# Kernel tuning notes

Measured on AMD Instinct MI355X. Metric: run time of the kernel, lower is better.

The kernel has to match this reference:

```python
import jax, jax.numpy as jnp
import numpy as np

N_NODES = 100000
K_NEIGH = 16
C = 128
B = 1


def setup_inputs() -> dict:
    key = jax.random.key(0)
    k1, k2, k3, k4, k5, k6 = jax.random.split(key, 6)
    inp = jax.random.normal(k1, (B, C, N_NODES), dtype=jnp.float32)
    adj = jax.random.randint(k2, (N_NODES, K_NEIGH), 0, N_NODES)
    w1 = jax.random.normal(k3, (C, C), dtype=jnp.float32) * 0.05
    b1 = jax.random.normal(k4, (C,), dtype=jnp.float32) * 0.05
    w2 = jax.random.normal(k5, (C, C), dtype=jnp.float32) * 0.05
    b2 = jax.random.normal(k6, (C,), dtype=jnp.float32) * 0.05
    return {"input": inp, "adj": adj, "w1": w1, "b1": b1, "w2": w2, "b2": b2}


def reference(input, adj, w1, b1, w2, b2):
    # fc1: 1x1 conv == channel-mixing matmul. input: [B, C, N]
    state_in = jnp.einsum('oc,bcn->bon', w1, input) + b1[None, :, None]
    # gather neighbor features: [B, C, N, K], mean over neighbors -> [B, C, N]
    neigh = input[:, :, adj]            # [B, C, N, K]
    agg = neigh.mean(axis=3)            # [B, C, N]
    fwd = jnp.einsum('oc,bcn->bon', w2, agg) + b2[None, :, None]
    return state_in + fwd
```

## Files before the change

### kernel.cpp

```cpp
#include <hip/hip_runtime.h>
#include <stdint.h>

#define N_NODES 100000
#define CH 128
#define K_NEIGH 16
#define TN 32
#define XT_STRIDE 36
#define XS_STRIDE 68
#define PS 132

#define PSWZ(n, o) ((n) * PS + ((o) ^ ((((n) >> 3) & 3) << 3)))


__device__ __forceinline__ uint32_t pack_bf16x2(float a, float b) {
    union { float f; uint32_t u; } ua, ub;
    ua.f = a; ub.f = b;
    const uint32_t ra = (ua.u + 0x7fffu + ((ua.u >> 16) & 1u)) >> 16;
    const uint32_t rb = (ub.u + 0x7fffu + ((ub.u >> 16) & 1u)) >> 16;
    return ra | (rb << 16);
}
__device__ __forceinline__ float bf16_lo(uint32_t u) {
    union { uint32_t u; float f; } c; c.u = u << 16; return c.f;
}
__device__ __forceinline__ float bf16_hi(uint32_t u) {
    union { uint32_t u; float f; } c; c.u = u & 0xffff0000u; return c.f;
}

__global__ __launch_bounds__(256, 8) void k_w2x_t(
    const float*  __restrict__ X,
    const float*  __restrict__ W2,
    uint16_t*     __restrict__ Yt)
{
    __shared__ __align__(16) float Xs[CH * XT_STRIDE];

    const int t  = threadIdx.x;
    const int n0 = blockIdx.x * TN;

    for (int it = 0; it < 4; ++it) {
        const int idx = t + it * 256;
        const int nq = idx & 7, c = idx >> 3;
        *(float4*)&Xs[c * XT_STRIDE + nq * 4] =
            *(const float4*)&X[(size_t)c * N_NODES + n0 + nq * 4];
    }
    __syncthreads();

    const int ng = t & 7, og = t >> 3;
    float acc[4][4];
#pragma unroll
    for (int i = 0; i < 4; ++i)
#pragma unroll
        for (int j = 0; j < 4; ++j) acc[i][j] = 0.0f;

    const float* wp = W2 + (size_t)(og * 4) * CH;
#pragma unroll 1
    for (int c0 = 0; c0 < CH; c0 += 4) {
        float4 wq[4];
#pragma unroll
        for (int i = 0; i < 4; ++i)
            wq[i] = *(const float4*)&wp[i * CH + c0];
#pragma unroll
        for (int e = 0; e < 4; ++e) {
            const float4 xv = *(const float4*)&Xs[(c0 + e) * XT_STRIDE + ng * 4];
#pragma unroll
            for (int i = 0; i < 4; ++i) {
                const float w = ((const float*)&wq[i])[e];
                acc[i][0] = fmaf(w, xv.x, acc[i][0]);
                acc[i][1] = fmaf(w, xv.y, acc[i][1]);
                acc[i][2] = fmaf(w, xv.z, acc[i][2]);
                acc[i][3] = fmaf(w, xv.w, acc[i][3]);
            }
        }
    }

#pragma unroll
    for (int j = 0; j < 4; ++j) {
        const int n = n0 + ng * 4 + j;
        uint2 v;
        v.x = pack_bf16x2(acc[0][j], acc[1][j]);
        v.y = pack_bf16x2(acc[2][j], acc[3][j]);
        *(uint2*)&Yt[(size_t)n * CH + og * 4] = v;
    }
}

__global__ __launch_bounds__(256, 8) void k_main(
    const float*    __restrict__ X,
    const int*      __restrict__ adj,
    const float*    __restrict__ W1,
    const float*    __restrict__ B1,
    const float*    __restrict__ B2,
    const uint16_t* __restrict__ Yt,
    float*          __restrict__ Out)
{
    __shared__ __align__(16) float Xs[CH * XT_STRIDE];
    __shared__ __align__(16) int adjS[TN * K_NEIGH];

    const int t  = threadIdx.x;
    const int n0 = blockIdx.x * TN;

    if (t < 128)
        *(int4*)&adjS[t * 4] = *(const int4*)&adj[(size_t)n0 * K_NEIGH + t * 4];
    for (int it = 0; it < 4; ++it) {
        const int idx = t + it * 256;
        const int nq = idx & 7, c = idx >> 3;
        *(float4*)&Xs[c * XT_STRIDE + nq * 4] =
            *(const float4*)&X[(size_t)c * N_NODES + n0 + nq * 4];
    }
    __syncthreads();

    const int ng = t & 7, og = t >> 3;
    float acc[4][4];
#pragma unroll
    for (int i = 0; i < 4; ++i)
#pragma unroll
        for (int j = 0; j < 4; ++j) acc[i][j] = 0.0f;

    const float* wp = W1 + (size_t)(og * 4) * CH;
#pragma unroll 1
    for (int c0 = 0; c0 < CH; c0 += 4) {
        float4 wq[4];
#pragma unroll
        for (int i = 0; i < 4; ++i)
            wq[i] = *(const float4*)&wp[i * CH + c0];
#pragma unroll
        for (int e = 0; e < 4; ++e) {
            const float4 xv = *(const float4*)&Xs[(c0 + e) * XT_STRIDE + ng * 4];
#pragma unroll
            for (int i = 0; i < 4; ++i) {
                const float w = ((const float*)&wq[i])[e];
                acc[i][0] = fmaf(w, xv.x, acc[i][0]);
                acc[i][1] = fmaf(w, xv.y, acc[i][1]);
                acc[i][2] = fmaf(w, xv.z, acc[i][2]);
                acc[i][3] = fmaf(w, xv.w, acc[i][3]);
            }
        }
    }

    __syncthreads();
    float* P = Xs;
#pragma unroll
    for (int j = 0; j < 4; ++j) {
        const int n = ng * 4 + j;
        float4 v = make_float4(acc[0][j], acc[1][j], acc[2][j], acc[3][j]);
        *(float4*)&P[PSWZ(n, og * 4)] = v;
    }
    __syncthreads();

    {
        const int l4 = (t & 31) * 4;
        const int g  = t >> 5;
        for (int itp = 0; itp < 4; ++itp) {
            const int n = itp * 8 + g;
            int js[K_NEIGH];
#pragma unroll
            for (int k = 0; k < K_NEIGH; ++k) js[k] = adjS[n * K_NEIGH + k];
            float4 a0 = make_float4(0.f, 0.f, 0.f, 0.f);
            float4 a1 = make_float4(0.f, 0.f, 0.f, 0.f);
#pragma unroll
            for (int k = 0; k < K_NEIGH; k += 2) {
                const uint2 v0 = *(const uint2*)&Yt[(size_t)js[k]     * CH + l4];
                const uint2 v1 = *(const uint2*)&Yt[(size_t)js[k + 1] * CH + l4];
                a0.x += bf16_lo(v0.x); a0.y += bf16_hi(v0.x);
                a0.z += bf16_lo(v0.y); a0.w += bf16_hi(v0.y);
                a1.x += bf16_lo(v1.x); a1.y += bf16_hi(v1.x);
                a1.z += bf16_lo(v1.y); a1.w += bf16_hi(v1.y);
            }
            float4 cur = *(const float4*)&P[PSWZ(n, l4)];
            cur.x += (a0.x + a1.x) * 0.0625f;
            cur.y += (a0.y + a1.y) * 0.0625f;
            cur.z += (a0.z + a1.z) * 0.0625f;
            cur.w += (a0.w + a1.w) * 0.0625f;
            *(float4*)&P[PSWZ(n, l4)] = cur;
        }
    }
    __syncthreads();

    for (int it = 0; it < 4; ++it) {
        const int idx = t + it * 256;
        const int o = idx >> 3, nq = idx & 7;
        const float bb = B1[o] + B2[o];
        float4 v;
        v.x = P[PSWZ(nq * 4 + 0, o)] + bb;
        v.y = P[PSWZ(nq * 4 + 1, o)] + bb;
        v.z = P[PSWZ(nq * 4 + 2, o)] + bb;
        v.w = P[PSWZ(nq * 4 + 3, o)] + bb;
        *(float4*)&Out[(size_t)o * N_NODES + n0 + nq * 4] = v;
    }
}

__global__ __launch_bounds__(256, 2) void k_fused_legacy(
    const float* __restrict__ X,
    const int*   __restrict__ adj,
    const float* __restrict__ W1,
    const float* __restrict__ B1,
    const float* __restrict__ W2,
    const float* __restrict__ B2,
    float*       __restrict__ Out)
{
    __shared__ __align__(16) float Xs[CH * XS_STRIDE];
    __shared__ __align__(16) float As[CH * XS_STRIDE];
    __shared__ int adjS[64 * K_NEIGH];

    const int t  = threadIdx.x;
    const int n0 = blockIdx.x * 64;
    const int V  = (N_NODES - n0 < 64) ? (N_NODES - n0) : 64;

    {
        const int base  = n0 * K_NEIGH;
        const int valid = V * K_NEIGH;
        for (int idx = t; idx < 64 * K_NEIGH; idx += 256)
            adjS[idx] = (idx < valid) ? adj[base + idx] : 0;
    }
    for (int it = 0; it < 32; ++it) {
        const int idx = t + it * 256;
        const int n = idx & 63, c = idx >> 6;
        Xs[c * XS_STRIDE + n] =
            (n < V) ? X[(size_t)c * N_NODES + n0 + n] : 0.0f;
    }
    __syncthreads();

    {
        const int n_l = t & 63, q = t >> 6;
        int js[K_NEIGH];
#pragma unroll
        for (int k = 0; k < K_NEIGH; ++k) js[k] = adjS[n_l * K_NEIGH + k];
        if (n_l < V) {
            for (int cc = 0; cc < 32; ++cc) {
                const int c = q * 32 + cc;
                const float* xc = X + (size_t)c * N_NODES;
                float s = 0.0f;
#pragma unroll
                for (int k = 0; k < K_NEIGH; ++k) s += xc[js[k]];
                As[c * XS_STRIDE + n_l] = s * 0.0625f;
            }
        } else {
            for (int cc = 0; cc < 32; ++cc)
                As[(q * 32 + cc) * XS_STRIDE + n_l] = 0.0f;
        }
    }
    __syncthreads();

    const int ng = t & 7, og = t >> 3;
    float acc[4][8];
#pragma unroll
    for (int i = 0; i < 4; ++i)
#pragma unroll
        for (int j = 0; j < 8; ++j) acc[i][j] = 0.0f;

    const float* w1p = W1 + (og * 4) * CH;
    const float* w2p = W2 + (og * 4) * CH;
    for (int c = 0; c < CH; ++c) {
        float xv[8], av[8], w1v[4], w2v[4];
        *(float4*)&xv[0] = *(const float4*)&Xs[c * XS_STRIDE + ng * 8];
        *(float4*)&xv[4] = *(const float4*)&Xs[c * XS_STRIDE + ng * 8 + 4];
        *(float4*)&av[0] = *(const float4*)&As[c * XS_STRIDE + ng * 8];
        *(float4*)&av[4] = *(const float4*)&As[c * XS_STRIDE + ng * 8 + 4];
#pragma unroll
        for (int i = 0; i < 4; ++i) {
            w1v[i] = w1p[i * CH + c];
            w2v[i] = w2p[i * CH + c];
        }
#pragma unroll
        for (int i = 0; i < 4; ++i)
#pragma unroll
            for (int j = 0; j < 8; ++j)
                acc[i][j] += w1v[i] * xv[j] + w2v[i] * av[j];
    }

    __syncthreads();
    float* Zt = Xs;
#pragma unroll
    for (int i = 0; i < 4; ++i) {
        *(float4*)&Zt[(og * 4 + i) * XS_STRIDE + ng * 8]     = *(float4*)&acc[i][0];
        *(float4*)&Zt[(og * 4 + i) * XS_STRIDE + ng * 8 + 4] = *(float4*)&acc[i][4];
    }
    __syncthreads();
    for (int it = 0; it < 32; ++it) {
        const int idx = t + it * 256;
        const int n = idx & 63, o = idx >> 6;
        if (n < V) {
            Out[(size_t)o * N_NODES + n0 + n] =
                Zt[o * XS_STRIDE + n] + B1[o] + B2[o];
        }
    }
}

extern "C" void kernel_launch(void* const* d_in, const int* in_sizes, int n_in,
                              void* d_out, int out_size, void* d_ws, size_t ws_size,
                              hipStream_t stream) {
    const float* X   = (const float*)d_in[0];
    const int*   adj = (const int*)d_in[1];
    const float* W1  = (const float*)d_in[2];
    const float* B1  = (const float*)d_in[3];
    const float* W2  = (const float*)d_in[4];
    const float* B2  = (const float*)d_in[5];
    float* Out = (float*)d_out;

    const size_t yt_bytes = (size_t)N_NODES * CH * sizeof(uint16_t);

    if (ws_size >= yt_bytes) {
        uint16_t* Yt = (uint16_t*)d_ws;
        const int nb = N_NODES / TN;
        k_w2x_t<<<nb, 256, 0, stream>>>(X, W2, Yt);
        k_main<<<nb, 256, 0, stream>>>(X, adj, W1, B1, B2, Yt, Out);
    } else {
        const int nblocks = (N_NODES + 63) / 64;
        k_fused_legacy<<<nblocks, 256, 0, stream>>>(X, adj, W1, B1, W2, B2, Out);
    }
}
```

Before: 281.9 us.

## Compute W2·X precompute with split-bf16 MFMA instead of scalar FP32 FMAs

Replaces the scalar FP32 W2·X precompute kernel with an MFMA-based kernel. W2 and X are each split into bf16 high and low parts, and three bf16 MFMAs approximate FP32 accuracy. A small kernel converts W2 into its hi/lo halves each call, and X is staged into swizzled shared memory as bf16 hi/lo. This aims to move the channel-mixing matmul onto the matrix cores. It adds an extra launch, extra workspace, and a lower occupancy bound of 2.

```diff
diff --git a/kernel.cpp b/kernel.cpp
--- a/kernel.cpp
+++ b/kernel.cpp
@@ -12,6 +12,9 @@
 #define PSWZ(n, o) ((n) * PS + ((o) ^ ((((n) >> 3) & 3) << 3)))
 
 
+typedef short bf8v __attribute__((ext_vector_type(8)));
+typedef float f32x4 __attribute__((ext_vector_type(4)));
+
 __device__ __forceinline__ uint32_t pack_bf16x2(float a, float b) {
     union { float f; uint32_t u; } ua, ub;
     ua.f = a; ub.f = b;
@@ -19,6 +22,13 @@
     const uint32_t rb = (ub.u + 0x7fffu + ((ub.u >> 16) & 1u)) >> 16;
     return ra | (rb << 16);
 }
+__device__ __forceinline__ uint16_t bf16_rne(float f) {
+    union { float f; uint32_t u; } c; c.f = f;
+    return (uint16_t)((c.u + 0x7fffu + ((c.u >> 16) & 1u)) >> 16);
+}
+__device__ __forceinline__ float bf16_tof(uint16_t h) {
+    union { uint32_t u; float f; } c; c.u = ((uint32_t)h) << 16; return c.f;
+}
 __device__ __forceinline__ float bf16_lo(uint32_t u) {
     union { uint32_t u; float f; } c; c.u = u << 16; return c.f;
 }
@@ -26,60 +36,104 @@
     union { uint32_t u; float f; } c; c.u = u & 0xffff0000u; return c.f;
 }
 
-__global__ __launch_bounds__(256, 8) void k_w2x_t(
-    const float*  __restrict__ X,
-    const float*  __restrict__ W2,
-    uint16_t*     __restrict__ Yt)
+__global__ void k_wcvt(const float* __restrict__ W,
+                       uint16_t* __restrict__ Wh, uint16_t* __restrict__ Wl) {
+    const int i = blockIdx.x * 256 + threadIdx.x;
+    if (i < CH * CH) {
+        const float f = W[i];
+        const uint16_t h = bf16_rne(f);
+        Wh[i] = h;
+        Wl[i] = bf16_rne(f - bf16_tof(h));
+    }
+}
+
+__global__ __launch_bounds__(256, 2) void k_w2x_mfma(
+    const float*    __restrict__ X,
+    const uint16_t* __restrict__ W2h,
+    const uint16_t* __restrict__ W2l,
+    uint16_t*       __restrict__ Yt)
 {
-    __shared__ __align__(16) float Xs[CH * XT_STRIDE];
+    __shared__ __align__(16) uint16_t XsH[64 * 128];
+    __shared__ __align__(16) uint16_t XsL[64 * 128];
 
     const int t  = threadIdx.x;
-    const int n0 = blockIdx.x * TN;
-
-    for (int it = 0; it < 4; ++it) {
-        const int idx = t + it * 256;
-        const int nq = idx & 7, c = idx >> 3;
-        *(float4*)&Xs[c * XT_STRIDE + nq * 4] =
-            *(const float4*)&X[(size_t)c * N_NODES + n0 + nq * 4];
-    }
-    __syncthreads();
-
-    const int ng = t & 7, og = t >> 3;
-    float acc[4][4];
-#pragma unroll
-    for (int i = 0; i < 4; ++i)
-#pragma unroll
-        for (int j = 0; j < 4; ++j) acc[i][j] = 0.0f;
-
-    const float* wp = W2 + (size_t)(og * 4) * CH;
-#pragma unroll 1
-    for (int c0 = 0; c0 < CH; c0 += 4) {
-        float4 wq[4];
-#pragma unroll
-        for (int i = 0; i < 4; ++i)
-            wq[i] = *(const float4*)&wp[i * CH + c0];
-#pragma unroll
-        for (int e = 0; e < 4; ++e) {
-            const float4 xv = *(const float4*)&Xs[(c0 + e) * XT_STRIDE + ng * 4];
-#pragma unroll
-            for (int i = 0; i < 4; ++i) {
-                const float w = ((const float*)&wq[i])[e];
-                acc[i][0] = fmaf(w, xv.x, acc[i][0]);
-                acc[i][1] = fmaf(w, xv.y, acc[i][1]);
-                acc[i][2] = fmaf(w, xv.z, acc[i][2]);
-                acc[i][3] = fmaf(w, xv.w, acc[i][3]);
-            }
-        }
-    }
-
-#pragma unroll
-    for (int j = 0; j < 4; ++j) {
-        const int n = n0 + ng * 4 + j;
-        uint2 v;
-        v.x = pack_bf16x2(acc[0][j], acc[1][j]);
-        v.y = pack_bf16x2(acc[2][j], acc[3][j]);
-        *(uint2*)&Yt[(size_t)n * CH + og * 4] = v;
-    }
+    const int n0 = blockIdx.x * 64;
+    const int V  = (N_NODES - n0 < 64) ? (N_NODES - n0) : 64;
+
+    for (int it = 0; it < 8; ++it) {
+        const int idx = t + it * 256;
+        const int nq = idx & 15, c = idx >> 4;
+        float4 v = make_float4(0.f, 0.f, 0.f, 0.f);
+        if (nq * 4 < V)
+            v = *(const float4*)&X[(size_t)c * N_NODES + n0 + nq * 4];
+        const float vv0 = v.x, vv1 = v.y, vv2 = v.z, vv3 = v.w;
+#pragma unroll
+        for (int s = 0; s < 4; ++s) {
+            const float f = (s == 0) ? vv0 : (s == 1) ? vv1 : (s == 2) ? vv2 : vv3;
+            const int n = nq * 4 + s;
+            const uint16_t h = bf16_rne(f);
+            const uint16_t lo = bf16_rne(f - bf16_tof(h));
+            const int byi = (n << 8) + (((c * 2)) ^ ((n & 7) << 4));
+            XsH[byi >> 1] = h;
+            XsL[byi >> 1] = lo;
+        }
+    }
+
+    const int l = t & 63;
+    const int w = t >> 6;
+    bf8v ah[2][4], al[2][4];
+    const int ar = l & 15;
+    const int ac = (l >> 4) * 8;
+#pragma unroll
+    for (int ot = 0; ot < 2; ++ot)
+#pragma unroll
+        for (int ks = 0; ks < 4; ++ks) {
+            const size_t off = (size_t)(w * 32 + ot * 16 + ar) * CH + ks * 32 + ac;
+            ah[ot][ks] = *(const bf8v*)&W2h[off];
+            al[ot][ks] = *(const bf8v*)&W2l[off];
+        }
+    __syncthreads();
+
+    f32x4 d[2][4];
+#pragma unroll
+    for (int ot = 0; ot < 2; ++ot)
+#pragma unroll
+        for (int nt = 0; nt < 4; ++nt)
+            d[ot][nt] = (f32x4){0.f, 0.f, 0.f, 0.f};
+
+#pragma unroll
+    for (int ks = 0; ks < 4; ++ks) {
+#pragma unroll
+        for (int nt = 0; nt < 4; ++nt) {
+            const int n  = nt * 16 + (l & 15);
+            const int byi = (n << 8) + ((ks * 64 + ((l >> 4) * 16)) ^ ((n & 7) << 4));
+            const bf8v bh = *(const bf8v*)((const char*)XsH + byi);
+            const bf8v bl = *(const bf8v*)((const char*)XsL + byi);
+#pragma unroll
+            for (int ot = 0; ot < 2; ++ot) {
+                d[ot][nt] = __builtin_amdgcn_mfma_f32_16x16x32_bf16(
+                    ah[ot][ks], bh, d[ot][nt], 0, 0, 0);
+                d[ot][nt] = __builtin_amdgcn_mfma_f32_16x16x32_bf16(
+                    al[ot][ks], bh, d[ot][nt], 0, 0, 0);
+                d[ot][nt] = __builtin_amdgcn_mfma_f32_16x16x32_bf16(
+                    ah[ot][ks], bl, d[ot][nt], 0, 0, 0);
+            }
+        }
+    }
+
+#pragma unroll
+    for (int ot = 0; ot < 2; ++ot)
+#pragma unroll
+        for (int nt = 0; nt < 4; ++nt) {
+            const int n = nt * 16 + (l & 15);
+            if (n < V) {
+                const int o4 = w * 32 + ot * 16 + (l >> 4) * 4;
+                uint2 pv;
+                pv.x = pack_bf16x2(d[ot][nt][0], d[ot][nt][1]);
+                pv.y = pack_bf16x2(d[ot][nt][2], d[ot][nt][3]);
+                *(uint2*)&Yt[(size_t)(n0 + n) * CH + o4] = pv;
+            }
+        }
 }
 
 __global__ __launch_bounds__(256, 8) void k_main(
@@ -296,12 +350,18 @@
     float* Out = (float*)d_out;
 
     const size_t yt_bytes = (size_t)N_NODES * CH * sizeof(uint16_t);
-
-    if (ws_size >= yt_bytes) {
-        uint16_t* Yt = (uint16_t*)d_ws;
-        const int nb = N_NODES / TN;
-        k_w2x_t<<<nb, 256, 0, stream>>>(X, W2, Yt);
-        k_main<<<nb, 256, 0, stream>>>(X, adj, W1, B1, B2, Yt, Out);
+    const size_t w_bytes  = (size_t)CH * CH * sizeof(uint16_t);
+    const size_t need     = yt_bytes + 2 * w_bytes;
+
+    if (ws_size >= need) {
+        uint16_t* Yt  = (uint16_t*)d_ws;
+        uint16_t* W2h = Yt + (size_t)N_NODES * CH;
+        uint16_t* W2l = W2h + (size_t)CH * CH;
+        k_wcvt<<<(CH * CH + 255) / 256, 256, 0, stream>>>(W2, W2h, W2l);
+        const int nb1 = (N_NODES + 63) / 64;
+        k_w2x_mfma<<<nb1, 256, 0, stream>>>(X, W2h, W2l, Yt);
+        const int nb2 = N_NODES / TN;
+        k_main<<<nb2, 256, 0, stream>>>(X, adj, W1, B1, B2, Yt, Out);
     } else {
         const int nblocks = (N_NODES + 63) / 64;
         k_fused_legacy<<<nblocks, 256, 0, stream>>>(X, adj, W1, B1, W2, B2, Out);
```

After: 248.9 us. -11.7%, faster.
